# Kernel tuning notes

Hardware: AMD Instinct MI355X
Metric: run time of the kernel (lower is better)

Reference implementation:

```python
import jax, jax.numpy as jnp
import numpy as np
from math import sqrt

D, H, B, L = 1024, 16, 2, 2048
DK = D // H

def linear(x, w, b):
    # torch Linear layout: w (out, in)
    return x @ w.T + b

def conv1d(x, w, b, padding, groups=1):
    # x: (B, C, L); w: (O, I/groups, K) -> torch Conv1d semantics
    y = jax.lax.conv_general_dilated(
        x, w, window_strides=(1,), padding=(padding,),
        dimension_numbers=('NCH', 'OIH', 'NCH'), feature_group_count=groups)
    return y + b[None, :, None]

def setup_inputs() -> dict:
    key = jax.random.key(0)
    ks = jax.random.split(key, 26)
    def n(k, shape, s=0.02):
        return jax.random.normal(k, shape, jnp.float32) * s
    return {
        'x': jax.random.normal(ks[0], (B, L, D), jnp.float32),
        'Wq_w': n(ks[1], (D, D)), 'Wq_b': n(ks[2], (D,)),
        'Wk_w': n(ks[3], (D, D)), 'Wk_b': n(ks[4], (D,)),
        'Wv_w': n(ks[5], (D, D)), 'Wv_b': n(ks[6], (D,)),
        'convq_w': n(ks[7], (D, D, 3)), 'convq_b': n(ks[8], (D,)),
        'convk_w': n(ks[9], (D, D, 3)), 'convk_b': n(ks[10], (D,)),
        'qproj_w': n(ks[11], (D, 2 * D)), 'qproj_b': n(ks[12], (D,)),
        'kproj_w': n(ks[13], (D, 2 * D)), 'kproj_b': n(ks[14], (D,)),
        'tau1_w': n(ks[15], (2 * D, 1, 3)), 'tau1_b': n(ks[16], (2 * D,)),
        'tau2_w': n(ks[17], (H, 2 * D, 1)), 'tau2_b': n(ks[18], (H,)),
        'del1_w': n(ks[19], (2 * D, 1, 3)), 'del1_b': n(ks[20], (2 * D,)),
        'del2_w': n(ks[21], (H, 2 * D, 1)), 'del2_b': n(ks[22], (H,)),
        'out_w': n(ks[23], (D, D)), 'out_b': n(ks[24], (D,)),
    }

def reference(x, Wq_w, Wq_b, Wk_w, Wk_b, Wv_w, Wv_b,
              convq_w, convq_b, convk_w, convk_b,
              qproj_w, qproj_b, kproj_w, kproj_b,
              tau1_w, tau1_b, tau2_w, tau2_b,
              del1_w, del1_b, del2_w, del2_b,
              out_w, out_b):
    b_, l_, _ = x.shape

    # Q branch: linear -> conv3 -> concat -> proj
    q_in = linear(x, Wq_w, Wq_b).transpose(0, 2, 1)          # (B, D, L)
    Q3 = conv1d(q_in, convq_w, convq_b, (1, 1))              # (B, D, L)
    Q_cat = jnp.concatenate([q_in, Q3], axis=1).transpose(0, 2, 1)  # (B, L, 2D)
    Q = linear(Q_cat, qproj_w, qproj_b).reshape(b_, l_, H, DK).transpose(0, 2, 1, 3)

    # K branch
    k_in = linear(x, Wk_w, Wk_b).transpose(0, 2, 1)
    K3 = conv1d(k_in, convk_w, convk_b, (1, 1))
    K_cat = jnp.concatenate([k_in, K3], axis=1).transpose(0, 2, 1)
    K = linear(K_cat, kproj_w, kproj_b).reshape(b_, l_, H, DK).transpose(0, 2, 1, 3)

    V = linear(x, Wv_w, Wv_b).reshape(b_, l_, H, DK).transpose(0, 2, 1, 3)

    # per-head tau (query-row scale) and delta (key-column bias), shape (B, H, L)
    x_conv = x.transpose(0, 2, 1)                             # (B, D, L)
    tau = jax.nn.sigmoid(conv1d(
        jax.nn.gelu(conv1d(x_conv, tau1_w, tau1_b, (1, 1), groups=D), approximate=False),
        tau2_w, tau2_b, (0, 0)))
    delta = jax.nn.sigmoid(conv1d(
        jax.nn.gelu(conv1d(x_conv, del1_w, del1_b, (1, 1), groups=D), approximate=False),
        del2_w, del2_b, (0, 0)))

    scores = jnp.einsum('bhqd,bhkd->bhqk', Q, K) / sqrt(DK)   # (B, H, L, L)
    scores = scores * tau[..., None] + delta[:, :, None, :]
    attn = jax.nn.softmax(scores, axis=-1)                    # dropout = identity (eval)
    out = jnp.einsum('bhqk,bhkd->bhqd', attn, V)
    out = out.transpose(0, 2, 1, 3).reshape(b_, l_, D)
    return linear(out, out_w, out_b)
```

## Files before the change

### kernel.cpp

```cpp
#include <hip/hip_runtime.h>

typedef __bf16 bf16_t;
typedef __bf16 bf16x8 __attribute__((ext_vector_type(8)));
typedef __bf16 bf16x4 __attribute__((ext_vector_type(4)));
typedef float f32x4 __attribute__((ext_vector_type(4)));

__device__ __forceinline__ void gload_lds16(const bf16_t* g, bf16_t* l) {
  __builtin_amdgcn_global_load_lds(
      (__attribute__((address_space(1))) void*)g,
      (__attribute__((address_space(3))) void*)l, 16, 0, 0);
}

__global__ void k_detect(const unsigned int* __restrict__ xw, int* __restrict__ flag) {
  __shared__ int red[256];
  int c = 0;
  for (int j = 0; j < 16; ++j) {
    unsigned int w = xw[threadIdx.x + (j << 8)];
    unsigned int e = (w >> 7) & 0xFF;
    c += (e >= 100 && e <= 150) ? 1 : 0;
  }
  red[threadIdx.x] = c;
  __syncthreads();
  for (int s = 128; s > 0; s >>= 1) {
    if (threadIdx.x < s) red[threadIdx.x] += red[threadIdx.x + s];
    __syncthreads();
  }
  if (threadIdx.x == 0) flag[0] = (red[0] > 2048) ? 1 : 0;
}

__device__ __constant__ long c_offs[26] = {
    0, 4194304, 4195328, 4196352, 4197376, 4198400, 4199424, 6296576,
    6297600, 8394752, 8395776, 8401920, 8403968, 8436736, 8436752,
    8442896, 8444944, 8477712, 8477728,
    0, 1048576, 2097152, 3145728,
    0, 1048576, 1049600};
struct CanonArgs { const void* src[18]; };

__global__ void k_canon(CanonArgs a, int base, int n, const int* __restrict__ flag,
                        bf16_t* __restrict__ dst) {
  long e0 = ((long)blockIdx.x * 256 + threadIdx.x) * 8;
  if (e0 >= c_offs[base + n]) return;
  int k = 0;
  while (e0 >= c_offs[base + k + 1]) ++k;
  const long rel = e0 - c_offs[base + k];
  if (flag[0]) {
    *(bf16x8*)&dst[e0] = *(const bf16x8*)((const bf16_t*)a.src[k] + rel);
  } else {
    const float* sf = (const float*)a.src[k] + rel;
    f32x4 lo = *(const f32x4*)sf;
    f32x4 hi = *(const f32x4*)(sf + 4);
    bf16x8 o;
    o[0] = (bf16_t)lo[0]; o[1] = (bf16_t)lo[1]; o[2] = (bf16_t)lo[2]; o[3] = (bf16_t)lo[3];
    o[4] = (bf16_t)hi[0]; o[5] = (bf16_t)hi[1]; o[6] = (bf16_t)hi[2]; o[7] = (bf16_t)hi[3];
    *(bf16x8*)&dst[e0] = o;
  }
}

__global__ void k_zero_pads(bf16_t* __restrict__ pad) {
  int idx = blockIdx.x * 256 + threadIdx.x;
  if (idx >= 8192) return;
  int b = idx >> 11;
  int r = (idx >> 10) & 1;
  int c = idx & 1023;
  long row = (long)b * 2050 + (r ? 2049 : 0);
  pad[row * 1024 + c] = (bf16_t)0.0f;
}

__global__ void k_convw_t2(const void* __restrict__ w0, const void* __restrict__ w1,
                           bf16_t* __restrict__ dst0, bf16_t* __restrict__ dst1,
                           const int* __restrict__ flag) {
  int idx = blockIdx.x * 256 + threadIdx.x;
  if (idx >= 6291456) return;
  const void* w = w0;
  bf16_t* dst = dst0;
  if (idx >= 3145728) { idx -= 3145728; w = w1; dst = dst1; }
  int o = idx / 3072;
  int rem = idx - o * 3072;
  int k = rem >> 10;
  int i = rem & 1023;
  int src = (o * 1024 + i) * 3 + k;
  float v = flag[0] ? (float)((const bf16_t*)w)[src] : ((const float*)w)[src];
  dst[idx] = (bf16_t)v;
}

struct GemmP {
  const bf16_t *A0, *A1;
  const bf16_t *B0, *B1, *B2;
  const bf16_t *bias0, *bias1, *bias2;
  bf16_t *C0, *C1, *C2;
  long a_jump, a1_jump;
  long cj0, cj1, cj2;
  int ksplit, lda, lda1, rpb, rpc, ldb, bsel_by_n, bshift, K, csel_by_n;
  int crs0, ccs0, crs1, ccs1, crs2, ccs2;
};

template <int BN, bool FINAL>
__global__ __launch_bounds__(256) void k_gemm(GemmP p, const int* __restrict__ flagp) {
  __shared__ __align__(16) bf16_t As[2][4096];
  __shared__ __align__(16) bf16_t Bs[2][BN * 32];
  const int tid = threadIdx.x;
  const int gx = gridDim.x;
  int lin = blockIdx.y * gx + blockIdx.x;
  const int nwg = gx * gridDim.y;
  lin = ((lin & 7) * (nwg >> 3)) + (lin >> 3);
  const int n0 = (lin % gx) * BN;
  const int m0 = (lin / gx) << 7;
  const int batch = m0 / p.rpb;
  const int cbatch = m0 / p.rpc;
  const int bidx = p.bsel_by_n ? (n0 >> 10) : (m0 >> p.bshift);
  const bf16_t* Bp = bidx == 0 ? p.B0 : (bidx == 1 ? p.B1 : p.B2);
  const bf16_t* biasp = bidx == 0 ? p.bias0 : (bidx == 1 ? p.bias1 : p.bias2);
  const long abase = (long)batch * p.a_jump;
  const long a1base = (long)cbatch * p.a1_jump;
  const int arow = tid >> 2;
  const int koff = (((tid & 3) ^ ((tid >> 3) & 3)) << 3);
  const int wid = tid >> 6, lane = tid & 63;
  const int l15 = lane & 15, lg = lane >> 4;
  const int nloc = n0 & 1023;

  constexpr int MI = (BN == 128) ? 4 : 2;
  const int wr = (BN == 128) ? ((wid >> 1) << 6) : (wid << 5);
  const int wc = (BN == 128) ? ((wid & 1) << 6) : 0;
  const int rsw = ((lg ^ (l15 >> 1)) & 3) << 3;

  f32x4 acc[MI][4];
#pragma unroll
  for (int i = 0; i < MI; ++i)
#pragma unroll
    for (int j = 0; j < 4; ++j) acc[i][j] = (f32x4){0.f, 0.f, 0.f, 0.f};

  auto stage = [&](int bufi, int k) {
    const int kg = k + koff;
#pragma unroll
    for (int half = 0; half < 2; ++half) {
      const int row = m0 + half * 64 + arow;
      const bf16_t* ap;
      if (kg < p.ksplit) ap = p.A0 + abase + (long)row * p.lda + kg;
      else               ap = p.A1 + a1base + (long)row * p.lda1 + (kg - p.ksplit);
      gload_lds16(ap, &As[bufi][half * 2048 + (tid << 3)]);
    }
    gload_lds16(Bp + (long)(nloc + arow) * p.ldb + kg, &Bs[bufi][tid << 3]);
    if (BN == 128)
      gload_lds16(Bp + (long)(nloc + 64 + arow) * p.ldb + kg, &Bs[bufi][2048 + (tid << 3)]);
  };

  const int nk = p.K >> 5;
  int buf = 0;
  stage(0, 0);
  for (int kt = 0; kt < nk; ++kt) {
    __syncthreads();
    if (kt + 1 < nk) stage(buf ^ 1, (kt + 1) << 5);
    bf16x8 af[MI], bfr[4];
#pragma unroll
    for (int i = 0; i < MI; ++i)
      af[i] = *(const bf16x8*)&As[buf][((wr + (i << 4) + l15) << 5) + rsw];
#pragma unroll
    for (int j = 0; j < 4; ++j)
      bfr[j] = *(const bf16x8*)&Bs[buf][((wc + (j << 4) + l15) << 5) + rsw];
#pragma unroll
    for (int i = 0; i < MI; ++i)
#pragma unroll
      for (int j = 0; j < 4; ++j)
        acc[i][j] = __builtin_amdgcn_mfma_f32_16x16x32_bf16(af[i], bfr[j], acc[i][j], 0, 0, 0);
    __syncthreads();
    buf ^= 1;
  }

  const int cp = p.csel_by_n ? (n0 >> 10) : (m0 >> p.bshift);
  bf16_t* Cb = cp == 0 ? p.C0 : (cp == 1 ? p.C1 : p.C2);
  const int crs = cp == 0 ? p.crs0 : (cp == 1 ? p.crs1 : p.crs2);
  const int ccs = cp == 0 ? p.ccs0 : (cp == 1 ? p.ccs1 : p.ccs2);
  const long cj = cp == 0 ? p.cj0 : (cp == 1 ? p.cj1 : p.cj2);
  const bool f32out = FINAL && (flagp[0] == 0);
  const long cbase = (long)batch * cj;
#pragma unroll
  for (int i = 0; i < MI; ++i) {
    const int row = m0 + wr + (i << 4) + (lg << 2);
#pragma unroll
    for (int j = 0; j < 4; ++j) {
      const int col = nloc + wc + (j << 4) + l15;
      const float bv = (float)biasp[col];
#pragma unroll
      for (int r = 0; r < 4; ++r) {
        const float val = acc[i][j][r] + bv;
        const long ci = cbase + (long)(row + r) * crs + (long)col * ccs;
        if (FINAL && f32out) ((float*)Cb)[ci] = val;
        else Cb[ci] = (bf16_t)val;
      }
    }
  }
}

__global__ __launch_bounds__(256) void k_taudelta(
    const bf16_t* __restrict__ x,
    const bf16_t* __restrict__ t1w, const bf16_t* __restrict__ t1b,
    const bf16_t* __restrict__ t2w, const bf16_t* __restrict__ t2b,
    const bf16_t* __restrict__ d1w, const bf16_t* __restrict__ d1b,
    const bf16_t* __restrict__ d2w, const bf16_t* __restrict__ d2b,
    float* __restrict__ tau, float* __restrict__ dlt)
{
  const int bt = blockIdx.x;
  const int t = bt & 2047;
  const int b = bt >> 11;
  const int tid = threadIdx.x;
  const bf16_t* xr = x + ((long)bt << 10);

  float acc[32];
#pragma unroll
  for (int i = 0; i < 32; ++i) acc[i] = 0.f;

  for (int j = 0; j < 8; ++j) {
    const int c = tid + (j << 8);
    const int src = c >> 1;
    const float x0 = (float)xr[src];
    const float xm = (t > 0) ? (float)xr[src - 1024] : 0.f;
    const float xp = (t < 2047) ? (float)xr[src + 1024] : 0.f;
    float st = (float)t1w[3 * c] * xm + (float)t1w[3 * c + 1] * x0 +
               (float)t1w[3 * c + 2] * xp + (float)t1b[c];
    float sd = (float)d1w[3 * c] * xm + (float)d1w[3 * c + 1] * x0 +
               (float)d1w[3 * c + 2] * xp + (float)d1b[c];
    const float gt = 0.5f * st * (1.f + erff(st * 0.70710678118f));
    const float gd = 0.5f * sd * (1.f + erff(sd * 0.70710678118f));
#pragma unroll
    for (int h = 0; h < 16; ++h) {
      acc[h]      += (float)t2w[(h << 11) + c] * gt;
      acc[16 + h] += (float)d2w[(h << 11) + c] * gd;
    }
  }

  __shared__ float red[256][33];
  __shared__ float red2[8][32];
#pragma unroll
  for (int i = 0; i < 32; ++i) red[tid][i] = acc[i];
  __syncthreads();
  const int i = tid & 31, g = tid >> 5;
  float p = 0.f;
#pragma unroll
  for (int k2 = 0; k2 < 32; ++k2) p += red[(g << 5) + k2][i];
  __syncthreads();
  red2[g][i] = p;
  __syncthreads();
  if (tid < 32) {
    float s = 0.f;
#pragma unroll
    for (int g2 = 0; g2 < 8; ++g2) s += red2[g2][tid];
    const int h = tid & 15;
    if (tid < 16) {
      s += (float)t2b[h];
      tau[((long)((b << 4) + h) << 11) + t] = 1.f / (1.f + __expf(-s));
    } else {
      s += (float)d2b[h];
      dlt[((long)((b << 4) + h) << 11) + t] =
          1.4426950408889634f / (1.f + __expf(-s));
    }
  }
}

__device__ __forceinline__ unsigned pk2(float a, float b) {
  union { bf16_t h[2]; unsigned u; } z;
  z.h[0] = (bf16_t)a; z.h[1] = (bf16_t)b;
  return z.u;
}

__global__ __launch_bounds__(256) void k_attn(
    const bf16_t* __restrict__ QKb, const bf16_t* __restrict__ VT,
    const float* __restrict__ tau, const float* __restrict__ dlt,
    bf16_t* __restrict__ O)
{
  const int lin = blockIdx.x;
  const int wg = ((lin & 7) << 7) + (lin >> 3);
  const int bh = wg >> 5, qt = wg & 31;
  const int tid = threadIdx.x;
  const int lane = tid & 63;
  const int wid = tid >> 6;
  const int l15 = lane & 15, lg = lane >> 4;
  const int b = bh >> 4, h = bh & 15;
  const int qbase = (qt << 6) + (wid << 4);

  const bf16_t* Qp = QKb + ((long)b << 21) + (h << 6);
  const bf16_t* Kp = QKb + 4194304 + ((long)b << 21) + (h << 6);
  const bf16_t* Vp = VT + ((long)bh << 17);
  const float* dltb = dlt + ((long)bh << 11);

  __shared__ __align__(16) bf16_t Ks[4096];
  __shared__ __align__(16) bf16_t Vs[4096];
  __shared__ unsigned Plds[4][16][32];

  bf16x8 qf[2];
#pragma unroll
  for (int kd = 0; kd < 2; ++kd)
    qf[kd] = *(const bf16x8*)&Qp[((long)(qbase + l15) << 10) + (kd << 5) + (lg << 3)];
  const float tq = tau[((long)bh << 11) + qbase + l15] * (0.125f * 1.4426950408889634f);

  bf16x8 onesf;
#pragma unroll
  for (int e = 0; e < 8; ++e) onesf[e] = (bf16_t)1.0f;

  f32x4 accO[4];
#pragma unroll
  for (int d = 0; d < 4; ++d) accO[d] = (f32x4){0.f, 0.f, 0.f, 0.f};
  f32x4 accL = (f32x4){0.f, 0.f, 0.f, 0.f};

  const int xr = (l15 & 7) << 2;

  for (int kk = 0; kk < 2048; kk += 64) {
    __syncthreads();
#pragma unroll
    for (int it = 0; it < 2; ++it) {
      const int t2 = tid + (it << 8);
      const int r = t2 >> 3, cc = (t2 & 7) ^ (r & 7);
      gload_lds16(Kp + ((long)(kk + r) << 10) + (cc << 3), &Ks[t2 << 3]);
    }
#pragma unroll
    for (int it = 0; it < 2; ++it) {
      const int t2 = tid + (it << 8);
      const int r = t2 >> 3;
      gload_lds16(Vp + ((long)r << 11) + kk + (((t2 & 7) ^ (r & 7)) << 3), &Vs[t2 << 3]);
    }
    __syncthreads();

    f32x4 st[4];
#pragma unroll
    for (int kb = 0; kb < 4; ++kb) {
      f32x4 z = (f32x4){0.f, 0.f, 0.f, 0.f};
#pragma unroll
      for (int kd = 0; kd < 2; ++kd) {
        const bf16x8 kf = *(const bf16x8*)&Ks[(((kb << 4) + l15) << 6) +
                                             ((((kd << 2) | lg) ^ (l15 & 7)) << 3)];
        z = __builtin_amdgcn_mfma_f32_16x16x32_bf16(kf, qf[kd], z, 0, 0, 0);
      }
      st[kb] = z;
    }

#pragma unroll
    for (int kb = 0; kb < 4; ++kb) {
      const f32x4 dl = *(const f32x4*)&dltb[kk + (kb << 4) + (lg << 2)];
      const float p0 = exp2f(fminf(fmaf(st[kb][0], tq, dl[0]), 30.f));
      const float p1 = exp2f(fminf(fmaf(st[kb][1], tq, dl[1]), 30.f));
      const float p2 = exp2f(fminf(fmaf(st[kb][2], tq, dl[2]), 30.f));
      const float p3 = exp2f(fminf(fmaf(st[kb][3], tq, dl[3]), 30.f));
      Plds[wid][l15][((kb << 3) + (lg << 1)) ^ xr]       = pk2(p0, p1);
      Plds[wid][l15][(((kb << 3) + (lg << 1)) | 1) ^ xr] = pk2(p2, p3);
    }
    asm volatile("s_waitcnt lgkmcnt(0)" ::: "memory");
    __builtin_amdgcn_sched_barrier(0);
    const bf16x8 pf0 = *(const bf16x8*)&Plds[wid][l15][(lg << 2) ^ xr];
    const bf16x8 pf1 = *(const bf16x8*)&Plds[wid][l15][(16 | (lg << 2)) ^ xr];
    asm volatile("s_waitcnt lgkmcnt(0)" ::: "memory");
    __builtin_amdgcn_sched_barrier(0);

#pragma unroll
    for (int d = 0; d < 4; ++d) {
      const bf16x8 vf0 = *(const bf16x8*)&Vs[(((d << 4) + l15) << 6) +
                                            ((lg ^ (l15 & 7)) << 3)];
      const bf16x8 vf1 = *(const bf16x8*)&Vs[(((d << 4) + l15) << 6) +
                                            (((4 | lg) ^ (l15 & 7)) << 3)];
      accO[d] = __builtin_amdgcn_mfma_f32_16x16x32_bf16(vf0, pf0, accO[d], 0, 0, 0);
      accO[d] = __builtin_amdgcn_mfma_f32_16x16x32_bf16(vf1, pf1, accO[d], 0, 0, 0);
    }
    accL = __builtin_amdgcn_mfma_f32_16x16x32_bf16(onesf, pf0, accL, 0, 0, 0);
    accL = __builtin_amdgcn_mfma_f32_16x16x32_bf16(onesf, pf1, accL, 0, 0, 0);
  }

  bf16_t* Ob = O + ((long)b << 21) + (h << 6);
  const float inv = 1.f / accL[0];
#pragma unroll
  for (int d = 0; d < 4; ++d) {
    bf16x4 ov;
#pragma unroll
    for (int r = 0; r < 4; ++r) ov[r] = (bf16_t)(accO[d][r] * inv);
    *(bf16x4*)&Ob[((long)(qbase + l15) << 10) + (d << 4) + (lg << 2)] = ov;
  }
}

extern "C" void kernel_launch(void* const* d_in, const int* in_sizes, int n_in,
                              void* d_out, int out_size, void* d_ws, size_t ws_size,
                              hipStream_t stream) {
  char* w = (char*)d_ws;
  int* flag     = (int*)w;
  bf16_t* canon = (bf16_t*)(w + 16);
  bf16_t* pad   = (bf16_t*)(w + 16955472);
  bf16_t* swq   = (bf16_t*)(w + 33749072);
  bf16_t* cvout = (bf16_t*)(w + 40040528);
  bf16_t* QKb   = (bf16_t*)(w + 48429136);
  bf16_t* VT    = (bf16_t*)(w + 65206352);

  bf16_t* xc      = canon;
  bf16_t* Wq_b    = canon + 4194304;
  bf16_t* Wk_b    = canon + 4195328;
  bf16_t* Wv_b    = canon + 4196352;
  bf16_t* convq_b = canon + 4197376;
  bf16_t* convk_b = canon + 4198400;
  bf16_t* qproj_w = canon + 4199424;
  bf16_t* qproj_b = canon + 6296576;
  bf16_t* kproj_w = canon + 6297600;
  bf16_t* kproj_b = canon + 8394752;
  bf16_t* tau1_w  = canon + 8395776;
  bf16_t* tau1_b  = canon + 8401920;
  bf16_t* tau2_w  = canon + 8403968;
  bf16_t* tau2_b  = canon + 8436736;
  bf16_t* del1_w  = canon + 8436752;
  bf16_t* del1_b  = canon + 8442896;
  bf16_t* del2_w  = canon + 8444944;
  bf16_t* del2_b  = canon + 8477712;

  bf16_t* pad_q = pad;
  bf16_t* Wq_w = swq, *Wk_w = swq + 1048576, *Wv_w = swq + 2097152;
  float* tau = (float*)swq;
  float* dlt = (float*)((char*)swq + 262144);
  bf16_t* convt_q = QKb;
  bf16_t* convt_k = QKb + 4194304;
  bf16_t* cv_q = xc;
  bf16_t* cv_k = cvout;
  bf16_t* outw_bf = pad;
  bf16_t* outb_bf = pad + 1048576;
  bf16_t* attn_out = xc;

  k_detect<<<1, 256, 0, stream>>>((const unsigned int*)d_in[0], flag);

  CanonArgs ca{};
  {
    const int idxA[18] = {0, 2, 4, 6, 8, 10, 11, 12, 13, 14,
                          15, 16, 17, 18, 19, 20, 21, 22};
    for (int i = 0; i < 18; ++i) ca.src[i] = d_in[idxA[i]];
    k_canon<<<4140, 256, 0, stream>>>(ca, 0, 18, flag, canon);
  }
  {
    CanonArgs cw{};
    cw.src[0] = d_in[1]; cw.src[1] = d_in[3]; cw.src[2] = d_in[5];
    k_canon<<<1536, 256, 0, stream>>>(cw, 19, 3, flag, swq);
  }
  k_zero_pads<<<32, 256, 0, stream>>>(pad);

  {
    GemmP p{};
    p.A0 = xc; p.A1 = xc;
    p.B0 = Wq_w; p.B1 = Wk_w; p.B2 = Wv_w;
    p.bias0 = Wq_b; p.bias1 = Wk_b; p.bias2 = Wv_b;
    p.C0 = pad_q + 1024; p.C1 = pad_q + 4198400 + 1024; p.C2 = VT;
    p.a_jump = 0; p.a1_jump = 0;
    p.cj0 = 2048; p.cj1 = 2048; p.cj2 = 2095104;
    p.ksplit = 1024; p.lda = 1024; p.lda1 = 1024; p.rpb = 2048; p.rpc = 4096;
    p.ldb = 1024; p.bsel_by_n = 1; p.bshift = 12; p.K = 1024; p.csel_by_n = 1;
    p.crs0 = 1024; p.ccs0 = 1; p.crs1 = 1024; p.ccs1 = 1; p.crs2 = 1; p.ccs2 = 2048;
    k_gemm<128, false><<<dim3(24, 32), 256, 0, stream>>>(p, flag);
  }

  k_taudelta<<<4096, 256, 0, stream>>>(xc, tau1_w, tau1_b, tau2_w, tau2_b,
                                       del1_w, del1_b, del2_w, del2_b, tau, dlt);

  k_convw_t2<<<24576, 256, 0, stream>>>(d_in[7], d_in[9], convt_q, convt_k, flag);

  {
    GemmP p{};
    p.A0 = pad; p.A1 = pad;
    p.B0 = convt_q; p.B1 = convt_k; p.B2 = convt_k;
    p.bias0 = convq_b; p.bias1 = convk_b; p.bias2 = convk_b;
    p.C0 = cv_q; p.C1 = cv_k - 4194304; p.C2 = cv_k;
    p.a_jump = 2048; p.a1_jump = 0;
    p.cj0 = 0; p.cj1 = 0; p.cj2 = 0;
    p.ksplit = 3072; p.lda = 1024; p.lda1 = 1024; p.rpb = 2048; p.rpc = 4096;
    p.ldb = 3072; p.bsel_by_n = 0; p.bshift = 12; p.K = 3072; p.csel_by_n = 0;
    p.crs0 = 1024; p.ccs0 = 1; p.crs1 = 1024; p.ccs1 = 1; p.crs2 = 1024; p.ccs2 = 1;
    k_gemm<128, false><<<dim3(8, 64), 256, 0, stream>>>(p, flag);
  }

  {
    GemmP p{};
    p.A0 = pad + 1024; p.A1 = cv_q;
    p.B0 = qproj_w; p.B1 = kproj_w; p.B2 = kproj_w;
    p.bias0 = qproj_b; p.bias1 = kproj_b; p.bias2 = kproj_b;
    p.C0 = QKb; p.C1 = QKb; p.C2 = QKb;
    p.a_jump = 2048;
    p.a1_jump = 20020256 - 4194304;
    p.cj0 = 0; p.cj1 = 0; p.cj2 = 0;
    p.ksplit = 1024; p.lda = 1024; p.lda1 = 1024; p.rpb = 2048; p.rpc = 4096;
    p.ldb = 2048; p.bsel_by_n = 0; p.bshift = 12; p.K = 2048; p.csel_by_n = 0;
    p.crs0 = 1024; p.ccs0 = 1; p.crs1 = 1024; p.ccs1 = 1; p.crs2 = 1024; p.ccs2 = 1;
    k_gemm<128, false><<<dim3(8, 64), 256, 0, stream>>>(p, flag);
  }

  {
    CanonArgs co{};
    co.src[0] = d_in[23]; co.src[1] = d_in[24];
    k_canon<<<513, 256, 0, stream>>>(co, 23, 2, flag, outw_bf);
  }

  k_attn<<<1024, 256, 0, stream>>>(QKb, VT, tau, dlt, attn_out);

  {
    GemmP p{};
    p.A0 = attn_out; p.A1 = attn_out;
    p.B0 = p.B1 = p.B2 = outw_bf;
    p.bias0 = p.bias1 = p.bias2 = outb_bf;
    p.C0 = p.C1 = p.C2 = (bf16_t*)d_out;
    p.a_jump = 0; p.a1_jump = 0;
    p.cj0 = p.cj1 = p.cj2 = 0;
    p.ksplit = 1024; p.lda = 1024; p.lda1 = 1024; p.rpb = 4096; p.rpc = 4096;
    p.ldb = 1024; p.bsel_by_n = 0; p.bshift = 12; p.K = 1024; p.csel_by_n = 0;
    p.crs0 = p.crs1 = p.crs2 = 1024; p.ccs0 = p.ccs1 = p.ccs2 = 1;
    k_gemm<64, true><<<dim3(16, 32), 256, 0, stream>>>(p, flag);
  }
}
```

Measured before the change: 410.5 us.

## Double-buffer K/V tiles in attention and use single barrier per GEMM iteration

```diff
diff --git a/kernel.cpp b/kernel.cpp
--- a/kernel.cpp
+++ b/kernel.cpp
@@ -147,8 +147,10 @@
   const int nk = p.K >> 5;
   int buf = 0;
   stage(0, 0);
+  asm volatile("s_waitcnt vmcnt(0)" ::: "memory");
+  __builtin_amdgcn_s_barrier();
+  __builtin_amdgcn_sched_barrier(0);
   for (int kt = 0; kt < nk; ++kt) {
-    __syncthreads();
     if (kt + 1 < nk) stage(buf ^ 1, (kt + 1) << 5);
     bf16x8 af[MI], bfr[4];
 #pragma unroll
@@ -162,7 +164,9 @@
 #pragma unroll
       for (int j = 0; j < 4; ++j)
         acc[i][j] = __builtin_amdgcn_mfma_f32_16x16x32_bf16(af[i], bfr[j], acc[i][j], 0, 0, 0);
-    __syncthreads();
+    if (kt + 1 < nk) asm volatile("s_waitcnt vmcnt(0)" ::: "memory");
+    __builtin_amdgcn_s_barrier();
+    __builtin_amdgcn_sched_barrier(0);
     buf ^= 1;
   }
 
@@ -282,8 +286,8 @@
   const bf16_t* Vp = VT + ((long)bh << 17);
   const float* dltb = dlt + ((long)bh << 11);
 
-  __shared__ __align__(16) bf16_t Ks[4096];
-  __shared__ __align__(16) bf16_t Vs[4096];
+  __shared__ __align__(16) bf16_t Ks[2][4096];
+  __shared__ __align__(16) bf16_t Vs[2][4096];
   __shared__ unsigned Plds[4][16][32];
 
   bf16x8 qf[2];
@@ -303,34 +307,44 @@
 
   const int xr = (l15 & 7) << 2;
 
-  for (int kk = 0; kk < 2048; kk += 64) {
-    __syncthreads();
+  auto stageKV = [&](int bufi, int kk) {
 #pragma unroll
     for (int it = 0; it < 2; ++it) {
       const int t2 = tid + (it << 8);
       const int r = t2 >> 3, cc = (t2 & 7) ^ (r & 7);
-      gload_lds16(Kp + ((long)(kk + r) << 10) + (cc << 3), &Ks[t2 << 3]);
+      gload_lds16(Kp + ((long)(kk + r) << 10) + (cc << 3), &Ks[bufi][t2 << 3]);
     }
 #pragma unroll
     for (int it = 0; it < 2; ++it) {
       const int t2 = tid + (it << 8);
       const int r = t2 >> 3;
-      gload_lds16(Vp + ((long)r << 11) + kk + (((t2 & 7) ^ (r & 7)) << 3), &Vs[t2 << 3]);
-    }
-    __syncthreads();
+      gload_lds16(Vp + ((long)r << 11) + kk + (((t2 & 7) ^ (r & 7)) << 3), &Vs[bufi][t2 << 3]);
+    }
+  };
+
+  int buf = 0;
+  stageKV(0, 0);
+  asm volatile("s_waitcnt vmcnt(0)" ::: "memory");
+  __builtin_amdgcn_s_barrier();
+  __builtin_amdgcn_sched_barrier(0);
+
+  for (int kk = 0; kk < 2048; kk += 64) {
+    if (kk + 64 < 2048) stageKV(buf ^ 1, kk + 64);
 
     f32x4 st[4];
+    __builtin_amdgcn_s_setprio(1);
 #pragma unroll
     for (int kb = 0; kb < 4; ++kb) {
       f32x4 z = (f32x4){0.f, 0.f, 0.f, 0.f};
 #pragma unroll
       for (int kd = 0; kd < 2; ++kd) {
-        const bf16x8 kf = *(const bf16x8*)&Ks[(((kb << 4) + l15) << 6) +
-                                             ((((kd << 2) | lg) ^ (l15 & 7)) << 3)];
+        const bf16x8 kf = *(const bf16x8*)&Ks[buf][(((kb << 4) + l15) << 6) +
+                                                  ((((kd << 2) | lg) ^ (l15 & 7)) << 3)];
         z = __builtin_amdgcn_mfma_f32_16x16x32_bf16(kf, qf[kd], z, 0, 0, 0);
       }
       st[kb] = z;
     }
+    __builtin_amdgcn_s_setprio(0);
 
 #pragma unroll
     for (int kb = 0; kb < 4; ++kb) {
@@ -349,17 +363,24 @@
     asm volatile("s_waitcnt lgkmcnt(0)" ::: "memory");
     __builtin_amdgcn_sched_barrier(0);
 
+    __builtin_amdgcn_s_setprio(1);
 #pragma unroll
     for (int d = 0; d < 4; ++d) {
-      const bf16x8 vf0 = *(const bf16x8*)&Vs[(((d << 4) + l15) << 6) +
-                                            ((lg ^ (l15 & 7)) << 3)];
-      const bf16x8 vf1 = *(const bf16x8*)&Vs[(((d << 4) + l15) << 6) +
-                                            (((4 | lg) ^ (l15 & 7)) << 3)];
+      const bf16x8 vf0 = *(const bf16x8*)&Vs[buf][(((d << 4) + l15) << 6) +
+                                                 ((lg ^ (l15 & 7)) << 3)];
+      const bf16x8 vf1 = *(const bf16x8*)&Vs[buf][(((d << 4) + l15) << 6) +
+                                                 (((4 | lg) ^ (l15 & 7)) << 3)];
       accO[d] = __builtin_amdgcn_mfma_f32_16x16x32_bf16(vf0, pf0, accO[d], 0, 0, 0);
       accO[d] = __builtin_amdgcn_mfma_f32_16x16x32_bf16(vf1, pf1, accO[d], 0, 0, 0);
     }
     accL = __builtin_amdgcn_mfma_f32_16x16x32_bf16(onesf, pf0, accL, 0, 0, 0);
     accL = __builtin_amdgcn_mfma_f32_16x16x32_bf16(onesf, pf1, accL, 0, 0, 0);
+    __builtin_amdgcn_s_setprio(0);
+
+    if (kk + 64 < 2048) asm volatile("s_waitcnt vmcnt(0)" ::: "memory");
+    __builtin_amdgcn_s_barrier();
+    __builtin_amdgcn_sched_barrier(0);
+    buf ^= 1;
   }
 
   bf16_t* Ob = O + ((long)b << 21) + (h << 6);
```

Result: no change. 410.7 us (+0.0%).
